# Kernel optimization log

Measured on AMD Instinct MI355X. Metric: run time of the kernel, lower is better.

Reference implementation:

```python
import jax, jax.numpy as jnp
import numpy as np

MAX_ONSET_DELAY_SAMPLES = 10


def apply_delays(templates, delays):
    # templates: (E, F, L), delays: (E, F) -> shifted templates with zero fill
    E, F, L = templates.shape
    d = jnp.round(jnp.clip(delays, -MAX_ONSET_DELAY_SAMPLES, MAX_ONSET_DELAY_SAMPLES)).astype(jnp.int32)
    idx = jnp.arange(L)                                   # (L,)
    src = idx[None, None, :] - d[:, :, None]              # (E, F, L) source index for torch.roll(shift=d)
    valid = (src >= 0) & (src < L)                        # zero out wrapped-around region
    src_c = jnp.clip(src, 0, L - 1)
    shifted = jnp.take_along_axis(templates, src_c, axis=2)
    return jnp.where(valid, shifted, jnp.zeros((), templates.dtype))


def setup_inputs() -> dict:
    key = jax.random.key(0)
    k1, k2, k3 = jax.random.split(key, 3)
    B, S, F = 64, 32768, 6
    E, L = 16, 80
    x = jax.random.normal(k1, (B, S, F), dtype=jnp.float32)
    templates = jax.random.normal(k2, (E, F, L), dtype=jnp.float32) * 0.1
    onset_delays = jax.random.normal(k3, (E, F), dtype=jnp.float32)
    return {"x": x, "templates": templates, "onset_delays": onset_delays}


def reference(x, templates, onset_delays):
    # x: (B, S, F); templates: (E, F, L); onset_delays: (E, F) -> scores (B, S, E)
    B, S, F = x.shape
    E, _, L = templates.shape
    delayed = apply_delays(templates, onset_delays)       # (E, F, L)
    kern = jnp.flip(delayed, axis=2)                      # torch flips template before conv1d
    pad = (L - 1) // 2
    # Fuse the 96 per-(event,feature) conv1d calls into one conv: sum over features
    # is exactly the input-channel contraction of a dense conv1d (in=F, out=E).
    score = jax.lax.conv_general_dilated(
        jnp.transpose(x, (0, 2, 1)),                      # (B, F, S)
        kern,                                             # (E, F, L) as OIH
        window_strides=(1,),
        padding=[(pad, pad)],
        dimension_numbers=("NCH", "OIH", "NCH"),
    )                                                     # (B, E, S_out)
    S_out = score.shape[2]
    if S_out > S:
        score = score[:, :, :S]
    elif S_out < S:
        score = jnp.pad(score, ((0, 0), (0, 0), (0, S - S_out)))
    return jnp.transpose(score, (0, 2, 1)) / (L * F)      # (B, S, E)
```

## Files before the change

### kernel.cpp

```cpp
#include <hip/hip_runtime.h>

#define BB 64
#define SS 32768
#define FF 6
#define EE 16
#define LL 80
#define KK 480
#define NSL 15
#define TBLK 256
#define NPHI 4
#define ROWS 64
#define WROW 336
#define WUNITS 166
#define WLDST 488

typedef _Float16 half8 __attribute__((ext_vector_type(8)));
typedef float f32x4 __attribute__((ext_vector_type(4)));

__global__ void prep_kernel(const float* __restrict__ tpl, const float* __restrict__ dly,
                            _Float16* __restrict__ wrev) {
    int n = blockIdx.x * 256 + threadIdx.x;
    if (n >= EE * KK) return;
    int e = n / KK, k = n - e * KK;
    int f = k / LL, r = k - f * LL;
    int m = LL - 1 - r;
    float dl = fminf(fmaxf(dly[e * FF + f], -10.f), 10.f);
    int d = (int)rintf(dl);
    int src = m - d;
    float v = (src >= 0 && src < LL) ? tpl[(e * FF + f) * LL + src] : 0.f;
    wrev[n] = (_Float16)v;
}

template <bool FROM_WS>
__global__ __launch_bounds__(512, 4) void corr_kernel(
    const float* __restrict__ x, const float* __restrict__ tpl,
    const float* __restrict__ dly, const _Float16* __restrict__ wrev,
    float* __restrict__ out) {
    __shared__ alignas(16) _Float16 Wlds[EE * WLDST];
    __shared__ alignas(16) _Float16 xs[NPHI][FF][WROW];

    int tid = threadIdx.x;
    int b = blockIdx.x >> 7;
    int t0 = (blockIdx.x & 127) << 8;

    if (FROM_WS) {
        for (int gi = tid; gi < EE * KK / 8; gi += 512) {
            int e = gi / 60;
            int k8 = (gi - e * 60) * 8;
            *(uint4*)&Wlds[e * WLDST + k8] = *(const uint4*)&wrev[e * KK + k8];
        }
    } else {
        for (int n = tid; n < EE * KK; n += 512) {
            int e = n / KK, k = n - e * KK;
            int f = k / LL, r = k - f * LL;
            int m = LL - 1 - r;
            float dl = fminf(fmaxf(dly[e * FF + f], -10.f), 10.f);
            int d = (int)rintf(dl);
            int src = m - d;
            float v = (src >= 0 && src < LL) ? tpl[(e * FF + f) * LL + src] : 0.f;
            Wlds[e * WLDST + k] = (_Float16)v;
        }
    }

    const float* xb = x + (size_t)b * (SS * FF);
    for (int it = tid; it < NPHI * WUNITS; it += 512) {
        int phi = it / WUNITS;
        int i = (it - phi * WUNITS) * 2;
        int pos = t0 + phi - 39 + i;
        float va[12];
        if (pos >= 0 && pos <= SS - 2) {
            const float* xp = xb + (size_t)pos * FF;
            #pragma unroll
            for (int q = 0; q < 6; q++)
                *(float2*)&va[2 * q] = *(const float2*)&xp[2 * q];
        } else {
            #pragma unroll
            for (int q = 0; q < 2; q++) {
                int p = pos + q;
                bool ok = (p >= 0) && (p < SS);
                #pragma unroll
                for (int f = 0; f < FF; f++)
                    va[q * 6 + f] = ok ? xb[(size_t)p * FF + f] : 0.f;
            }
        }
        #pragma unroll
        for (int f = 0; f < FF; f++) {
#if __has_builtin(__builtin_amdgcn_cvt_pkrtz)
            __fp16 __attribute__((ext_vector_type(2))) hp =
                __builtin_amdgcn_cvt_pkrtz(va[f], va[6 + f]);
            *(decltype(hp)*)&xs[phi][f][i] = hp;
#else
            xs[phi][f][i] = (_Float16)va[f];
            xs[phi][f][i + 1] = (_Float16)va[6 + f];
#endif
        }
    }
    __syncthreads();

    int lane = tid & 63;
    int wid = tid >> 6;
    int e = lane & 15;
    int g = lane >> 4;
    int phi = wid & 3;
    int pairi = wid >> 2;

    half8 bq[NSL];
    #pragma unroll
    for (int s = 0; s < NSL; s++)
        bq[s] = *(const half8*)&Wlds[e * WLDST + 32 * s + 8 * g];

    const char* xph = (const char*)&xs[phi][0][0];
    f32x4 acc[2];
    #pragma unroll
    for (int tt = 0; tt < 2; tt++) acc[tt] = (f32x4){0.f, 0.f, 0.f, 0.f};

    #pragma unroll
    for (int tt = 0; tt < 2; tt++) {
        int R = pairi * 32 + tt * 16 + (lane & 15);
        #pragma unroll
        for (int s = 0; s < NSL; s++) {
            int k0 = 32 * s + 8 * g;
            int f = (k0 * 205) >> 14;
            int r0 = k0 - 80 * f;
            const char* p = xph + 2 * (f * WROW + 4 * R + r0);
            uint2 lo = *(const uint2*)p;
            uint2 hi = *(const uint2*)(p + 8);
            union { unsigned u[4]; half8 h; } av;
            av.u[0] = lo.x; av.u[1] = lo.y; av.u[2] = hi.x; av.u[3] = hi.y;
            acc[tt] = __builtin_amdgcn_mfma_f32_16x16x32_f16(av.h, bq[s], acc[tt], 0, 0, 0);
        }
    }

    #pragma unroll
    for (int tt = 0; tt < 2; tt++) {
        #pragma unroll
        for (int j = 0; j < 4; j++) {
            int row = pairi * 32 + tt * 16 + g * 4 + j;
            int t = t0 + phi + 4 * row;
            float v = acc[tt][j] * (1.0f / 480.0f);
            if (t == SS - 1) v = 0.f;
            out[((size_t)b * SS + t) * EE + e] = v;
        }
    }
}

extern "C" void kernel_launch(void* const* d_in, const int* in_sizes, int n_in,
                              void* d_out, int out_size, void* d_ws, size_t ws_size,
                              hipStream_t stream) {
    const float* x = (const float*)d_in[0];
    const float* tpl = (const float*)d_in[1];
    const float* dly = (const float*)d_in[2];
    float* out = (float*)d_out;

    int grid = BB * (SS / TBLK);
    if (ws_size >= (size_t)(EE * KK * sizeof(_Float16))) {
        _Float16* wrev = (_Float16*)d_ws;
        prep_kernel<<<(EE * KK + 255) / 256, 256, 0, stream>>>(tpl, dly, wrev);
        corr_kernel<true><<<grid, 512, 0, stream>>>(x, tpl, dly, wrev, out);
    } else {
        corr_kernel<false><<<grid, 512, 0, stream>>>(x, tpl, dly, nullptr, out);
    }
}
```

Measured before the change: 66.98 us.

## Load MFMA B-fragments directly from global and halve block size

The weight fragments are now read straight from the workspace buffer into registers instead of being staged through a shared-memory copy. That removes the LDS weight tile and the store-then-load round trip on the default path. Blocks shrink from 512 to 256 threads, and each wave now covers four 16-row tiles of one phase instead of two. The x staging row is trimmed to 332 halves, which cuts LDS use per block and is meant to allow more resident blocks. The trade-off is more global/L2 traffic for weights, since every wave fetches them separately, and less parallelism per block.

```diff
diff --git a/kernel.cpp b/kernel.cpp
--- a/kernel.cpp
+++ b/kernel.cpp
@@ -9,10 +9,8 @@
 #define NSL 15
 #define TBLK 256
 #define NPHI 4
-#define ROWS 64
-#define WROW 336
+#define WROW 332
 #define WUNITS 166
-#define WLDST 488
 
 typedef _Float16 half8 __attribute__((ext_vector_type(8)));
 typedef float f32x4 __attribute__((ext_vector_type(4)));
@@ -32,38 +30,46 @@
 }
 
 template <bool FROM_WS>
-__global__ __launch_bounds__(512, 4) void corr_kernel(
+__global__ __launch_bounds__(256, 8) void corr_kernel(
     const float* __restrict__ x, const float* __restrict__ tpl,
     const float* __restrict__ dly, const _Float16* __restrict__ wrev,
     float* __restrict__ out) {
-    __shared__ alignas(16) _Float16 Wlds[EE * WLDST];
     __shared__ alignas(16) _Float16 xs[NPHI][FF][WROW];
 
     int tid = threadIdx.x;
     int b = blockIdx.x >> 7;
     int t0 = (blockIdx.x & 127) << 8;
 
-    if (FROM_WS) {
-        for (int gi = tid; gi < EE * KK / 8; gi += 512) {
-            int e = gi / 60;
-            int k8 = (gi - e * 60) * 8;
-            *(uint4*)&Wlds[e * WLDST + k8] = *(const uint4*)&wrev[e * KK + k8];
-        }
+    int lane = tid & 63;
+    int wid = tid >> 6;
+    int e = lane & 15;
+    int g = lane >> 4;
+
+    half8 bq[NSL];
+    if constexpr (FROM_WS) {
+        #pragma unroll
+        for (int s = 0; s < NSL; s++)
+            bq[s] = *(const half8*)&wrev[e * KK + 32 * s + 8 * g];
     } else {
-        for (int n = tid; n < EE * KK; n += 512) {
-            int e = n / KK, k = n - e * KK;
+        __shared__ _Float16 Wlds[EE * KK];
+        for (int n = tid; n < EE * KK; n += 256) {
+            int ee = n / KK, k = n - ee * KK;
             int f = k / LL, r = k - f * LL;
             int m = LL - 1 - r;
-            float dl = fminf(fmaxf(dly[e * FF + f], -10.f), 10.f);
+            float dl = fminf(fmaxf(dly[ee * FF + f], -10.f), 10.f);
             int d = (int)rintf(dl);
             int src = m - d;
-            float v = (src >= 0 && src < LL) ? tpl[(e * FF + f) * LL + src] : 0.f;
-            Wlds[e * WLDST + k] = (_Float16)v;
+            float v = (src >= 0 && src < LL) ? tpl[(ee * FF + f) * LL + src] : 0.f;
+            Wlds[n] = (_Float16)v;
         }
+        __syncthreads();
+        #pragma unroll
+        for (int s = 0; s < NSL; s++)
+            bq[s] = *(const half8*)&Wlds[e * KK + 32 * s + 8 * g];
     }
 
     const float* xb = x + (size_t)b * (SS * FF);
-    for (int it = tid; it < NPHI * WUNITS; it += 512) {
+    for (int it = tid; it < NPHI * WUNITS; it += 256) {
         int phi = it / WUNITS;
         int i = (it - phi * WUNITS) * 2;
         int pos = t0 + phi - 39 + i;
@@ -97,26 +103,15 @@
     }
     __syncthreads();
 
-    int lane = tid & 63;
-    int wid = tid >> 6;
-    int e = lane & 15;
-    int g = lane >> 4;
-    int phi = wid & 3;
-    int pairi = wid >> 2;
-
-    half8 bq[NSL];
+    int phi = wid;
+    const char* xph = (const char*)&xs[phi][0][0];
+    f32x4 acc[4];
     #pragma unroll
-    for (int s = 0; s < NSL; s++)
-        bq[s] = *(const half8*)&Wlds[e * WLDST + 32 * s + 8 * g];
-
-    const char* xph = (const char*)&xs[phi][0][0];
-    f32x4 acc[2];
-    #pragma unroll
-    for (int tt = 0; tt < 2; tt++) acc[tt] = (f32x4){0.f, 0.f, 0.f, 0.f};
+    for (int tt = 0; tt < 4; tt++) acc[tt] = (f32x4){0.f, 0.f, 0.f, 0.f};
 
     #pragma unroll
-    for (int tt = 0; tt < 2; tt++) {
-        int R = pairi * 32 + tt * 16 + (lane & 15);
+    for (int tt = 0; tt < 4; tt++) {
+        int R = tt * 16 + (lane & 15);
         #pragma unroll
         for (int s = 0; s < NSL; s++) {
             int k0 = 32 * s + 8 * g;
@@ -132,10 +127,10 @@
     }
 
     #pragma unroll
-    for (int tt = 0; tt < 2; tt++) {
+    for (int tt = 0; tt < 4; tt++) {
         #pragma unroll
         for (int j = 0; j < 4; j++) {
-            int row = pairi * 32 + tt * 16 + g * 4 + j;
+            int row = tt * 16 + g * 4 + j;
             int t = t0 + phi + 4 * row;
             float v = acc[tt][j] * (1.0f / 480.0f);
             if (t == SS - 1) v = 0.f;
@@ -156,8 +151,8 @@
     if (ws_size >= (size_t)(EE * KK * sizeof(_Float16))) {
         _Float16* wrev = (_Float16*)d_ws;
         prep_kernel<<<(EE * KK + 255) / 256, 256, 0, stream>>>(tpl, dly, wrev);
-        corr_kernel<true><<<grid, 512, 0, stream>>>(x, tpl, dly, wrev, out);
+        corr_kernel<true><<<grid, 256, 0, stream>>>(x, tpl, dly, wrev, out);
     } else {
-        corr_kernel<false><<<grid, 512, 0, stream>>>(x, tpl, dly, nullptr, out);
+        corr_kernel<false><<<grid, 256, 0, stream>>>(x, tpl, dly, nullptr, out);
     }
 }
```

New measurement: 118.0 us. 76.2% more time.
